# Performance work log

Measured on AMD Instinct MI355X. Metric: run time of the kernel, lower is better.

The kernel has to match this reference:

```python
import jax, jax.numpy as jnp
import numpy as np

H = 8          # number of heads
D_MODEL = 512  # model dim
D_HEAD = D_MODEL // H


def setup_inputs() -> dict:
    key = jax.random.key(0)
    ks = jax.random.split(key, 8)
    B, C, L = 4, D_MODEL, 2048
    s = 1.0 / np.sqrt(D_MODEL)
    return {
        "x1": jax.random.normal(ks[0], (B, C, L), dtype=jnp.float32),
        "x2": jax.random.normal(ks[1], (B, C, L), dtype=jnp.float32),
        "Wq": jax.random.uniform(ks[2], (D_MODEL, D_MODEL), jnp.float32, -s, s),
        "bq": jax.random.uniform(ks[3], (D_MODEL,), jnp.float32, -s, s),
        "Wk": jax.random.uniform(ks[4], (D_MODEL, D_MODEL), jnp.float32, -s, s),
        "bk": jax.random.uniform(ks[5], (D_MODEL,), jnp.float32, -s, s),
        "Wv": jax.random.uniform(ks[6], (D_MODEL, D_MODEL), jnp.float32, -s, s),
        "bv": jax.random.uniform(ks[7], (D_MODEL,), jnp.float32, -s, s),
    }


def reference(x1, x2, Wq, bq, Wk, bk, Wv, bv):
    # x1, x2: [B, C, L] with C == d_model (3D branch of the torch module)
    B, C, L = x1.shape
    x1t = jnp.swapaxes(x1, 1, 2)  # [B, L, C]
    x2t = jnp.swapaxes(x2, 1, 2)  # [B, L, C]

    def proj(x, W, b):  # torch Linear: x @ W.T + b, then split heads
        y = jnp.einsum('blc,dc->bld', x, W) + b          # [B, L, C]
        return y.reshape(B, -1, H, D_HEAD).transpose(0, 2, 1, 3)  # [B, H, L, d]

    q = proj(x1t, Wq, bq)
    k = proj(x2t, Wk, bk)
    v = proj(x2t, Wv, bv)

    scores = jnp.einsum('bhqd,bhkd->bhqk', q, k) / jnp.sqrt(
        jnp.asarray(D_HEAD, dtype=q.dtype))
    attn = jax.nn.softmax(scores, axis=-1)
    out = jnp.einsum('bhqk,bhkd->bhqd', attn, v)          # [B, H, L, d]

    # transpose(1,2).view(B,-1,C).transpose(1,2) -> [B, C, L]
    out = out.transpose(0, 2, 1, 3).reshape(B, L, C)
    return jnp.swapaxes(out, 1, 2)
```

## Files before the change

### kernel.cpp

```cpp
#include <hip/hip_runtime.h>
#include <hip/hip_bf16.h>

#define L_SEQ 2048
#define DM 512
#define NB 4

typedef short bf16x8 __attribute__((ext_vector_type(8)));
typedef float f32x4 __attribute__((ext_vector_type(4)));
typedef unsigned short u16;
typedef u16 u16x8 __attribute__((ext_vector_type(8)));
typedef u16 u16x4 __attribute__((ext_vector_type(4)));

__device__ __forceinline__ u16 f2bf(float f) {
    unsigned int u = __float_as_uint(f);
    u += 0x7fffu + ((u >> 16) & 1u);
    return (u16)(u >> 16);
}

__device__ __forceinline__ unsigned int pk_bf16(float a, float b) {
    __hip_bfloat162 h = __float22bfloat162_rn(float2{a, b});
    unsigned int u;
    __builtin_memcpy(&u, &h, 4);
    return u;
}

__device__ __forceinline__ void lds_load16(const void* g, void* l) {
    __builtin_amdgcn_global_load_lds(
        (const __attribute__((address_space(1))) unsigned int*)g,
        (__attribute__((address_space(3))) unsigned int*)l,
        16, 0, 0);
}

__global__ void cvt_w(const float* __restrict__ Wq, const float* __restrict__ Wk,
                      const float* __restrict__ Wv, u16* __restrict__ dst) {
    int i = blockIdx.x * blockDim.x + threadIdx.x;
    int which = i >> 16, j = i & 65535;
    const float* src = (which == 0) ? Wq : (which == 1 ? Wk : Wv);
    float4 v = ((const float4*)src)[j];
    ushort4 o;
    o.x = f2bf(v.x); o.y = f2bf(v.y); o.z = f2bf(v.z); o.w = f2bf(v.w);
    ((ushort4*)dst)[i] = o;
}

__global__ void tr_cvt_x(const float* __restrict__ x1, const float* __restrict__ x2,
                         u16* __restrict__ dst) {
    __shared__ float t[64][69];
    const int z = blockIdx.z, b = z & 3, c0 = blockIdx.y * 64, l0 = blockIdx.x * 64;
    const float* src = (z < 4) ? x1 : x2;
    u16* dbase = dst + (size_t)(z >> 2) * 4194304;
    const int tid = threadIdx.x;
    const float* sp = src + ((size_t)b * DM + c0) * L_SEQ + l0;
#pragma unroll
    for (int p = 0; p < 4; ++p) {
        int id = p * 256 + tid;
        int ci = id >> 4, lj = (id & 15) * 4;
        float4 v = *(const float4*)(sp + (size_t)ci * L_SEQ + lj);
        t[ci][lj] = v.x; t[ci][lj + 1] = v.y; t[ci][lj + 2] = v.z; t[ci][lj + 3] = v.w;
    }
    __syncthreads();
    u16* dp = dbase + ((size_t)b * L_SEQ + l0) * DM + c0;
#pragma unroll
    for (int p = 0; p < 2; ++p) {
        int id = p * 256 + tid;
        int lj = id >> 3, c8 = (id & 7) * 8;
        u16x8 o;
#pragma unroll
        for (int i = 0; i < 8; ++i) o[i] = f2bf(t[c8 + i][lj]);
        *(u16x8*)(dp + (size_t)lj * DM + c8) = o;
    }
}

__launch_bounds__(256, 2)
__global__ void proj_gemm(const u16* __restrict__ x1T, const u16* __restrict__ x2T,
                          const u16* __restrict__ Wall,
                          const float* __restrict__ bq, const float* __restrict__ bk,
                          const float* __restrict__ bv,
                          u16* __restrict__ Qo, u16* __restrict__ Ko, u16* __restrict__ Vto) {
    __shared__ __align__(16) char smem[34816];
    u16* a_lds = (u16*)smem;
    u16* b_lds = (u16*)(smem + 8192);
    const int by = blockIdx.y;
    const int b = by / 3, pj = by % 3;
    const int m0 = (blockIdx.x >> 2) * 128, n0 = (blockIdx.x & 3) * 128;
    const u16* xT = (pj == 0) ? x1T : x2T;
    const u16* W = Wall + (size_t)pj * 262144;
    const float* bias = (pj == 0) ? bq : (pj == 1 ? bk : bv);
    const float scale = (pj == 0) ? 0.18033688011112042f : 1.0f;

    const int tid = threadIdx.x;
    const int w = tid >> 6, lane = tid & 63;
    const int lm = lane & 15, lq = lane >> 4;
    const int wrow = (w & 1) * 64, wcol = (w >> 1) * 64;

    const u16* gsrc[4];
    u16* ldst[4];
#pragma unroll
    for (int j = 0; j < 4; ++j) {
        int s = (j & 1) * 256 + w * 64 + lane;
        int r = s >> 2, c = s & 3, cc = c ^ (r & 3);
        if (j < 2) {
            gsrc[j] = xT + ((size_t)b * L_SEQ + m0 + r) * DM + cc * 8;
            ldst[j] = a_lds + ((j & 1) * 256 + w * 64) * 8;
        } else {
            gsrc[j] = W + (size_t)(n0 + r) * DM + cc * 8;
            ldst[j] = b_lds + ((j & 1) * 256 + w * 64) * 8;
        }
    }

    f32x4 acc[4][4];
#pragma unroll
    for (int mt = 0; mt < 4; ++mt)
#pragma unroll
        for (int nt = 0; nt < 4; ++nt) acc[mt][nt] = (f32x4){0.f, 0.f, 0.f, 0.f};

    for (int kt = 0; kt < 16; ++kt) {
        __syncthreads();
#pragma unroll
        for (int j = 0; j < 4; ++j) lds_load16(gsrc[j] + kt * 32, ldst[j]);
        __syncthreads();
        bf16x8 af[4], bfr[4];
#pragma unroll
        for (int mt = 0; mt < 4; ++mt) {
            int r = wrow + mt * 16 + lm;
            int ch = lq ^ (r & 3);
            af[mt] = *(const bf16x8*)(a_lds + r * 32 + ch * 8);
        }
#pragma unroll
        for (int nt = 0; nt < 4; ++nt) {
            int r = wcol + nt * 16 + lm;
            int ch = lq ^ (r & 3);
            bfr[nt] = *(const bf16x8*)(b_lds + r * 32 + ch * 8);
        }
#pragma unroll
        for (int mt = 0; mt < 4; ++mt)
#pragma unroll
            for (int nt = 0; nt < 4; ++nt)
                acc[mt][nt] = __builtin_amdgcn_mfma_f32_16x16x32_bf16(af[mt], bfr[nt], acc[mt][nt], 0, 0, 0);
    }

    float bvv[4];
#pragma unroll
    for (int nt = 0; nt < 4; ++nt) bvv[nt] = bias[n0 + wcol + nt * 16 + lm];

    if (pj < 2) {
        u16* dst = (pj == 0) ? Qo : Ko;
#pragma unroll
        for (int mt = 0; mt < 4; ++mt)
#pragma unroll
            for (int nt = 0; nt < 4; ++nt) {
                int col = n0 + wcol + nt * 16 + lm;
#pragma unroll
                for (int r = 0; r < 4; ++r) {
                    int row = m0 + wrow + mt * 16 + lq * 4 + r;
                    dst[((size_t)b * L_SEQ + row) * DM + col] = f2bf((acc[mt][nt][r] + bvv[nt]) * scale);
                }
            }
    } else {
        __syncthreads();
        u16* epi = (u16*)smem;
#pragma unroll
        for (int mt = 0; mt < 4; ++mt)
#pragma unroll
            for (int nt = 0; nt < 4; ++nt) {
                int colL = wcol + nt * 16 + lm;
                int row0 = wrow + mt * 16 + lq * 4;
                u16x4 tv;
#pragma unroll
                for (int r = 0; r < 4; ++r) tv[r] = f2bf(acc[mt][nt][r] + bvv[nt]);
                *(u16x4*)(epi + colL * 136 + row0) = tv;
            }
        __syncthreads();
#pragma unroll
        for (int p = 0; p < 8; ++p) {
            int id = p * 256 + tid;
            int rr = id >> 4, ch = id & 15;
            u16x8 vv = *(const u16x8*)(epi + rr * 136 + ch * 8);
            *(u16x8*)(Vto + ((size_t)b * DM + n0 + rr) * L_SEQ + m0 + ch * 8) = vv;
        }
    }
}

__launch_bounds__(512, 4)
__global__ void attn(const u16* __restrict__ Q, const u16* __restrict__ K,
                     const u16* __restrict__ Vt, float* __restrict__ out) {
    __shared__ __align__(16) char smem[66048];
    u16* k_lds = (u16*)smem;
    u16* v_lds = (u16*)(smem + 16384);
    u16* p_lds = (u16*)(smem + 32768);
    float* o_lds = (float*)(smem + 32768);
    float* l_lds = (float*)(smem + 65536);

    const int qb = blockIdx.x, h = blockIdx.y, b = blockIdx.z;
    const int tid = threadIdx.x, w = tid >> 6, lane = tid & 63;
    const int q0 = qb * 128, wr = w * 16;
    const int lm = lane & 15, lq = lane >> 4;

    const u16* Qb = Q + ((size_t)b * L_SEQ + q0) * DM + h * 64;
    const u16* Kb = K + (size_t)b * L_SEQ * DM + h * 64;
    const u16* Vb = Vt + ((size_t)b * DM + h * 64) * L_SEQ;

    const u16 *gQ[2], *gK[2], *gV[2];
    u16 *dK[2], *dV[2];
#pragma unroll
    for (int j = 0; j < 2; ++j) {
        int s = j * 512 + w * 64 + lane;
        int r = s >> 3, c = s & 7, cc = c ^ (r & 7);
        gQ[j] = Qb + (size_t)r * DM + cc * 8;
        gK[j] = Kb + (size_t)r * DM + cc * 8;
        dK[j] = k_lds + (j * 512 + w * 64) * 8;
        int d = s >> 4, kc = s & 15, kcc = kc ^ (d & 15);
        gV[j] = Vb + (size_t)d * L_SEQ + kcc * 8;
        dV[j] = v_lds + (j * 512 + w * 64) * 8;
    }

#pragma unroll
    for (int j = 0; j < 2; ++j) lds_load16(gQ[j], dK[j]);
    __syncthreads();
    bf16x8 qf[2];
#pragma unroll
    for (int kb = 0; kb < 2; ++kb) {
        int r = wr + lm;
        int ch = (kb * 4 + lq) ^ (r & 7);
        qf[kb] = *(const bf16x8*)(k_lds + r * 64 + ch * 8);
    }

    float l_part = 0.f;
    f32x4 o_acc[4];
#pragma unroll
    for (int dt = 0; dt < 4; ++dt) o_acc[dt] = (f32x4){0.f, 0.f, 0.f, 0.f};

    for (int kt = 0; kt < 16; ++kt) {
        __syncthreads();
#pragma unroll
        for (int j = 0; j < 2; ++j) lds_load16(gK[j] + (size_t)kt * 128 * DM, dK[j]);
#pragma unroll
        for (int j = 0; j < 2; ++j) lds_load16(gV[j] + kt * 128, dV[j]);
        __syncthreads();

#pragma unroll
        for (int nt = 0; nt < 8; ++nt) {
            int rk = nt * 16 + lm;
            bf16x8 kf0 = *(const bf16x8*)(k_lds + rk * 64 + ((0 + lq) ^ (rk & 7)) * 8);
            bf16x8 kf1 = *(const bf16x8*)(k_lds + rk * 64 + ((4 + lq) ^ (rk & 7)) * 8);
            f32x4 s = (f32x4){0.f, 0.f, 0.f, 0.f};
            s = __builtin_amdgcn_mfma_f32_16x16x32_bf16(kf0, qf[0], s, 0, 0, 0);
            s = __builtin_amdgcn_mfma_f32_16x16x32_bf16(kf1, qf[1], s, 0, 0, 0);
            float p0 = __builtin_amdgcn_exp2f(s[0]);
            float p1 = __builtin_amdgcn_exp2f(s[1]);
            float p2 = __builtin_amdgcn_exp2f(s[2]);
            float p3 = __builtin_amdgcn_exp2f(s[3]);
            l_part += (p0 + p1) + (p2 + p3);
            unsigned int w0 = pk_bf16(p0, p1), w1 = pk_bf16(p2, p3);
            int q = wr + lm;
            int c8 = nt * 2 + (lq >> 1);
            int chs = c8 ^ (q & 15);
            uint2 pw; pw.x = w0; pw.y = w1;
            *(uint2*)(p_lds + q * 128 + chs * 8 + (lq & 1) * 4) = pw;
        }

#pragma unroll
        for (int kb = 0; kb < 4; ++kb) {
            int r = wr + lm;
            int ch = (kb * 4 + lq) ^ (r & 15);
            bf16x8 pf = *(const bf16x8*)(p_lds + r * 128 + ch * 8);
#pragma unroll
            for (int dt = 0; dt < 4; ++dt) {
                int d = dt * 16 + lm;
                int chv = (kb * 4 + lq) ^ (d & 15);
                bf16x8 vf = *(const bf16x8*)(v_lds + d * 128 + chv * 8);
                o_acc[dt] = __builtin_amdgcn_mfma_f32_16x16x32_bf16(pf, vf, o_acc[dt], 0, 0, 0);
            }
        }
    }

    l_part += __shfl_xor(l_part, 16);
    l_part += __shfl_xor(l_part, 32);

    __syncthreads();
    if (lq == 0) l_lds[wr + lm] = 1.0f / l_part;
    {
        int row0 = wr + lq * 4;
        int rc = row0 >> 2;
#pragma unroll
        for (int dt = 0; dt < 4; ++dt) {
            int col = dt * 16 + lm;
            *(f32x4*)(o_lds + col * 128 + ((rc ^ (col & 31)) << 2)) = o_acc[dt];
        }
    }
    __syncthreads();
    float* ob = out + ((size_t)b * DM + h * 64) * L_SEQ + q0;
#pragma unroll
    for (int p = 0; p < 4; ++p) {
        int id = p * 512 + tid;
        int d = id >> 5, rc = id & 31;
        f32x4 vv = *(const f32x4*)(o_lds + d * 128 + ((rc ^ (d & 31)) << 2));
        f32x4 il = *(const f32x4*)(l_lds + rc * 4);
#pragma unroll
        for (int j = 0; j < 4; ++j) vv[j] *= il[j];
        *(f32x4*)(ob + (size_t)d * L_SEQ + rc * 4) = vv;
    }
}

extern "C" void kernel_launch(void* const* d_in, const int* in_sizes, int n_in,
                              void* d_out, int out_size, void* d_ws, size_t ws_size,
                              hipStream_t stream) {
    const float* x1 = (const float*)d_in[0];
    const float* x2 = (const float*)d_in[1];
    const float* Wq = (const float*)d_in[2];
    const float* bq = (const float*)d_in[3];
    const float* Wk = (const float*)d_in[4];
    const float* bk = (const float*)d_in[5];
    const float* Wv = (const float*)d_in[6];
    const float* bv = (const float*)d_in[7];
    float* out = (float*)d_out;

    char* ws = (char*)d_ws;
    u16* x1T = (u16*)(ws);
    u16* x2T = (u16*)(ws + 8388608);
    u16* Wall = (u16*)(ws + 16777216);
    u16* Qb  = (u16*)(ws + 18350080);
    u16* Kb  = (u16*)(ws + 26738688);
    u16* Vtb = (u16*)(ws + 35127296);

    cvt_w<<<768, 256, 0, stream>>>(Wq, Wk, Wv, Wall);
    tr_cvt_x<<<dim3(32, 8, 8), 256, 0, stream>>>(x1, x2, x1T);
    proj_gemm<<<dim3(64, 12), 256, 0, stream>>>(x1T, x2T, Wall, bq, bk, bv, Qb, Kb, Vtb);
    attn<<<dim3(16, 8, 4), 512, 0, stream>>>(Qb, Kb, Vtb, out);
}
```

Before: 164.4 us.

## Double-buffer GEMM and attention tiles, stage Q/K epilogue, enlarge transpose tiles

The projection GEMM and the attention kernel now double-buffer their LDS tiles, issuing the next tile's loads before computing on the current one, so each iteration needs one barrier instead of two. Attention switches to 64-key tiles with a smaller LDS footprint and remaps blocks over a linear grid for locality. The Q/K GEMM epilogue goes through LDS to produce coalesced 16-byte stores instead of scattered 2-byte writes. The transpose-convert kernel uses 128x128 tiles and converts to bf16 before staging, which halves shared memory traffic. The cost is more LDS per block and more iterations with shorter bodies in attention, which may affect occupancy and latency hiding.

Measured after the change: 174.6 us. 1.06x slower.

```diff
diff --git a/kernel.cpp b/kernel.cpp
--- a/kernel.cpp
+++ b/kernel.cpp
@@ -3,7 +3,6 @@
 
 #define L_SEQ 2048
 #define DM 512
-#define NB 4
 
 typedef short bf16x8 __attribute__((ext_vector_type(8)));
 typedef float f32x4 __attribute__((ext_vector_type(4)));
@@ -44,41 +43,41 @@
 
 __global__ void tr_cvt_x(const float* __restrict__ x1, const float* __restrict__ x2,
                          u16* __restrict__ dst) {
-    __shared__ float t[64][69];
-    const int z = blockIdx.z, b = z & 3, c0 = blockIdx.y * 64, l0 = blockIdx.x * 64;
+    __shared__ u16 t[128 * 136];
+    const int z = blockIdx.z, b = z & 3, c0 = blockIdx.y * 128, l0 = blockIdx.x * 128;
     const float* src = (z < 4) ? x1 : x2;
     u16* dbase = dst + (size_t)(z >> 2) * 4194304;
     const int tid = threadIdx.x;
     const float* sp = src + ((size_t)b * DM + c0) * L_SEQ + l0;
 #pragma unroll
-    for (int p = 0; p < 4; ++p) {
+    for (int p = 0; p < 16; ++p) {
         int id = p * 256 + tid;
-        int ci = id >> 4, lj = (id & 15) * 4;
-        float4 v = *(const float4*)(sp + (size_t)ci * L_SEQ + lj);
-        t[ci][lj] = v.x; t[ci][lj + 1] = v.y; t[ci][lj + 2] = v.z; t[ci][lj + 3] = v.w;
+        int ci = id >> 5, f4 = id & 31;
+        float4 v = *(const float4*)(sp + (size_t)ci * L_SEQ + f4 * 4);
+        u16x4 o;
+        o[0] = f2bf(v.x); o[1] = f2bf(v.y); o[2] = f2bf(v.z); o[3] = f2bf(v.w);
+        *(u16x4*)(t + ci * 136 + f4 * 4) = o;
     }
     __syncthreads();
     u16* dp = dbase + ((size_t)b * L_SEQ + l0) * DM + c0;
 #pragma unroll
-    for (int p = 0; p < 2; ++p) {
+    for (int p = 0; p < 8; ++p) {
         int id = p * 256 + tid;
-        int lj = id >> 3, c8 = (id & 7) * 8;
+        int lj = id >> 4, c8 = id & 15;
         u16x8 o;
 #pragma unroll
-        for (int i = 0; i < 8; ++i) o[i] = f2bf(t[c8 + i][lj]);
-        *(u16x8*)(dp + (size_t)lj * DM + c8) = o;
-    }
-}
-
-__launch_bounds__(256, 2)
+        for (int i = 0; i < 8; ++i) o[i] = t[(c8 * 8 + i) * 136 + lj];
+        *(u16x8*)(dp + (size_t)lj * DM + c8 * 8) = o;
+    }
+}
+
+__launch_bounds__(256, 3)
 __global__ void proj_gemm(const u16* __restrict__ x1T, const u16* __restrict__ x2T,
                           const u16* __restrict__ Wall,
                           const float* __restrict__ bq, const float* __restrict__ bk,
                           const float* __restrict__ bv,
                           u16* __restrict__ Qo, u16* __restrict__ Ko, u16* __restrict__ Vto) {
     __shared__ __align__(16) char smem[34816];
-    u16* a_lds = (u16*)smem;
-    u16* b_lds = (u16*)(smem + 8192);
     const int by = blockIdx.y;
     const int b = by / 3, pj = by % 3;
     const int m0 = (blockIdx.x >> 2) * 128, n0 = (blockIdx.x & 3) * 128;
@@ -92,19 +91,15 @@
     const int lm = lane & 15, lq = lane >> 4;
     const int wrow = (w & 1) * 64, wcol = (w >> 1) * 64;
 
-    const u16* gsrc[4];
-    u16* ldst[4];
-#pragma unroll
-    for (int j = 0; j < 4; ++j) {
-        int s = (j & 1) * 256 + w * 64 + lane;
+    const u16* gA[2]; const u16* gB[2];
+    int adst[2];
+#pragma unroll
+    for (int j = 0; j < 2; ++j) {
+        int s = j * 256 + tid;
         int r = s >> 2, c = s & 3, cc = c ^ (r & 3);
-        if (j < 2) {
-            gsrc[j] = xT + ((size_t)b * L_SEQ + m0 + r) * DM + cc * 8;
-            ldst[j] = a_lds + ((j & 1) * 256 + w * 64) * 8;
-        } else {
-            gsrc[j] = W + (size_t)(n0 + r) * DM + cc * 8;
-            ldst[j] = b_lds + ((j & 1) * 256 + w * 64) * 8;
-        }
+        gA[j] = xT + ((size_t)b * L_SEQ + m0 + r) * DM + cc * 8;
+        gB[j] = W + (size_t)(n0 + r) * DM + cc * 8;
+        adst[j] = (j * 256 + w * 64) * 8;
     }
 
     f32x4 acc[4][4];
@@ -112,24 +107,35 @@
     for (int mt = 0; mt < 4; ++mt)
 #pragma unroll
         for (int nt = 0; nt < 4; ++nt) acc[mt][nt] = (f32x4){0.f, 0.f, 0.f, 0.f};
+
+#pragma unroll
+    for (int j = 0; j < 2; ++j) {
+        lds_load16(gA[j], (u16*)smem + adst[j]);
+        lds_load16(gB[j], (u16*)(smem + 8192) + adst[j]);
+    }
 
     for (int kt = 0; kt < 16; ++kt) {
         __syncthreads();
-#pragma unroll
-        for (int j = 0; j < 4; ++j) lds_load16(gsrc[j] + kt * 32, ldst[j]);
-        __syncthreads();
+        if (kt < 15) {
+            int nb = (kt + 1) & 1;
+#pragma unroll
+            for (int j = 0; j < 2; ++j) {
+                lds_load16(gA[j] + (kt + 1) * 32, (u16*)(smem + nb * 16384) + adst[j]);
+                lds_load16(gB[j] + (kt + 1) * 32, (u16*)(smem + 8192 + nb * 16384) + adst[j]);
+            }
+        }
+        const u16* a_lds = (const u16*)(smem + (kt & 1) * 16384);
+        const u16* b_lds = (const u16*)(smem + 8192 + (kt & 1) * 16384);
         bf16x8 af[4], bfr[4];
 #pragma unroll
         for (int mt = 0; mt < 4; ++mt) {
             int r = wrow + mt * 16 + lm;
-            int ch = lq ^ (r & 3);
-            af[mt] = *(const bf16x8*)(a_lds + r * 32 + ch * 8);
+            af[mt] = *(const bf16x8*)(a_lds + r * 32 + (lq ^ (r & 3)) * 8);
         }
 #pragma unroll
         for (int nt = 0; nt < 4; ++nt) {
             int r = wcol + nt * 16 + lm;
-            int ch = lq ^ (r & 3);
-            bfr[nt] = *(const bf16x8*)(b_lds + r * 32 + ch * 8);
+            bfr[nt] = *(const bf16x8*)(b_lds + r * 32 + (lq ^ (r & 3)) * 8);
         }
 #pragma unroll
         for (int mt = 0; mt < 4; ++mt)
@@ -142,34 +148,32 @@
 #pragma unroll
     for (int nt = 0; nt < 4; ++nt) bvv[nt] = bias[n0 + wcol + nt * 16 + lm];
 
+    __syncthreads();
+    u16* epi = (u16*)smem;
+#pragma unroll
+    for (int mt = 0; mt < 4; ++mt)
+#pragma unroll
+        for (int nt = 0; nt < 4; ++nt) {
+            int colL = wcol + nt * 16 + lm;
+            int row0 = wrow + mt * 16 + lq * 4;
+            u16x4 tv;
+#pragma unroll
+            for (int r = 0; r < 4; ++r) tv[r] = f2bf((acc[mt][nt][r] + bvv[nt]) * scale);
+            *(u16x4*)(epi + colL * 136 + row0) = tv;
+        }
+    __syncthreads();
     if (pj < 2) {
         u16* dst = (pj == 0) ? Qo : Ko;
 #pragma unroll
-        for (int mt = 0; mt < 4; ++mt)
-#pragma unroll
-            for (int nt = 0; nt < 4; ++nt) {
-                int col = n0 + wcol + nt * 16 + lm;
-#pragma unroll
-                for (int r = 0; r < 4; ++r) {
-                    int row = m0 + wrow + mt * 16 + lq * 4 + r;
-                    dst[((size_t)b * L_SEQ + row) * DM + col] = f2bf((acc[mt][nt][r] + bvv[nt]) * scale);
-                }
-            }
+        for (int p = 0; p < 8; ++p) {
+            int id = p * 256 + tid;
+            int lj = id >> 4, c8 = id & 15;
+            u16x8 o;
+#pragma unroll
+            for (int i = 0; i < 8; ++i) o[i] = epi[(c8 * 8 + i) * 136 + lj];
+            *(u16x8*)(dst + ((size_t)b * L_SEQ + m0 + lj) * DM + n0 + c8 * 8) = o;
+        }
     } else {
-        __syncthreads();
-        u16* epi = (u16*)smem;
-#pragma unroll
-        for (int mt = 0; mt < 4; ++mt)
-#pragma unroll
-            for (int nt = 0; nt < 4; ++nt) {
-                int colL = wcol + nt * 16 + lm;
-                int row0 = wrow + mt * 16 + lq * 4;
-                u16x4 tv;
-#pragma unroll
-                for (int r = 0; r < 4; ++r) tv[r] = f2bf(acc[mt][nt][r] + bvv[nt]);
-                *(u16x4*)(epi + colL * 136 + row0) = tv;
-            }
-        __syncthreads();
 #pragma unroll
         for (int p = 0; p < 8; ++p) {
             int id = p * 256 + tid;
@@ -183,14 +187,16 @@
 __launch_bounds__(512, 4)
 __global__ void attn(const u16* __restrict__ Q, const u16* __restrict__ K,
                      const u16* __restrict__ Vt, float* __restrict__ out) {
-    __shared__ __align__(16) char smem[66048];
-    u16* k_lds = (u16*)smem;
-    u16* v_lds = (u16*)(smem + 16384);
+    __shared__ __align__(16) char smem[49664];
     u16* p_lds = (u16*)(smem + 32768);
-    float* o_lds = (float*)(smem + 32768);
-    float* l_lds = (float*)(smem + 65536);
-
-    const int qb = blockIdx.x, h = blockIdx.y, b = blockIdx.z;
+    float* l_lds = (float*)(smem + 49152);
+    float* o_lds = (float*)smem;
+
+    const int i = blockIdx.x;
+    const int g = i & 7, r_ = i >> 3;
+    const int qb = r_ & 15, bh = ((r_ >> 4) << 3) + g;
+    const int h = bh >> 2, b = bh & 3;
+
     const int tid = threadIdx.x, w = tid >> 6, lane = tid & 63;
     const int q0 = qb * 128, wr = w * 16;
     const int lm = lane & 15, lq = lane >> 4;
@@ -199,49 +205,55 @@
     const u16* Kb = K + (size_t)b * L_SEQ * DM + h * 64;
     const u16* Vb = Vt + ((size_t)b * DM + h * 64) * L_SEQ;
 
-    const u16 *gQ[2], *gK[2], *gV[2];
-    u16 *dK[2], *dV[2];
+    const u16 *gK, *gV;
+    int sdst;
+    {
+        int r = tid >> 3, c = tid & 7, cc = c ^ (r & 7);
+        gK = Kb + (size_t)r * DM + cc * 8;
+        gV = Vb + (size_t)r * L_SEQ + cc * 8;
+        sdst = (w * 64) * 8;
+    }
+
 #pragma unroll
     for (int j = 0; j < 2; ++j) {
-        int s = j * 512 + w * 64 + lane;
+        int s = j * 512 + tid;
         int r = s >> 3, c = s & 7, cc = c ^ (r & 7);
-        gQ[j] = Qb + (size_t)r * DM + cc * 8;
-        gK[j] = Kb + (size_t)r * DM + cc * 8;
-        dK[j] = k_lds + (j * 512 + w * 64) * 8;
-        int d = s >> 4, kc = s & 15, kcc = kc ^ (d & 15);
-        gV[j] = Vb + (size_t)d * L_SEQ + kcc * 8;
-        dV[j] = v_lds + (j * 512 + w * 64) * 8;
-    }
-
-#pragma unroll
-    for (int j = 0; j < 2; ++j) lds_load16(gQ[j], dK[j]);
+        lds_load16(Qb + (size_t)r * DM + cc * 8, (u16*)(smem + j * 8192) + sdst);
+    }
     __syncthreads();
     bf16x8 qf[2];
 #pragma unroll
     for (int kb = 0; kb < 2; ++kb) {
         int r = wr + lm;
-        int ch = (kb * 4 + lq) ^ (r & 7);
-        qf[kb] = *(const bf16x8*)(k_lds + r * 64 + ch * 8);
-    }
+        const u16* qsrc = (const u16*)(smem + (r >> 6) * 8192)
+                          + (r & 63) * 64 + ((kb * 4 + lq) ^ (r & 7)) * 8;
+        qf[kb] = *(const bf16x8*)qsrc;
+    }
+    __syncthreads();
 
     float l_part = 0.f;
     f32x4 o_acc[4];
 #pragma unroll
     for (int dt = 0; dt < 4; ++dt) o_acc[dt] = (f32x4){0.f, 0.f, 0.f, 0.f};
 
-    for (int kt = 0; kt < 16; ++kt) {
+    lds_load16(gK, (u16*)smem + sdst);
+    lds_load16(gV, (u16*)(smem + 16384) + sdst);
+
+    for (int kt = 0; kt < 32; ++kt) {
         __syncthreads();
-#pragma unroll
-        for (int j = 0; j < 2; ++j) lds_load16(gK[j] + (size_t)kt * 128 * DM, dK[j]);
-#pragma unroll
-        for (int j = 0; j < 2; ++j) lds_load16(gV[j] + kt * 128, dV[j]);
-        __syncthreads();
-
-#pragma unroll
-        for (int nt = 0; nt < 8; ++nt) {
+        if (kt < 31) {
+            int nb = (kt + 1) & 1;
+            lds_load16(gK + (size_t)(kt + 1) * 64 * DM, (u16*)(smem + nb * 8192) + sdst);
+            lds_load16(gV + (kt + 1) * 64, (u16*)(smem + 16384 + nb * 8192) + sdst);
+        }
+        const u16* kl = (const u16*)(smem + (kt & 1) * 8192);
+        const u16* vl = (const u16*)(smem + 16384 + (kt & 1) * 8192);
+
+#pragma unroll
+        for (int nt = 0; nt < 4; ++nt) {
             int rk = nt * 16 + lm;
-            bf16x8 kf0 = *(const bf16x8*)(k_lds + rk * 64 + ((0 + lq) ^ (rk & 7)) * 8);
-            bf16x8 kf1 = *(const bf16x8*)(k_lds + rk * 64 + ((4 + lq) ^ (rk & 7)) * 8);
+            bf16x8 kf0 = *(const bf16x8*)(kl + rk * 64 + ((0 + lq) ^ (rk & 7)) * 8);
+            bf16x8 kf1 = *(const bf16x8*)(kl + rk * 64 + ((4 + lq) ^ (rk & 7)) * 8);
             f32x4 s = (f32x4){0.f, 0.f, 0.f, 0.f};
             s = __builtin_amdgcn_mfma_f32_16x16x32_bf16(kf0, qf[0], s, 0, 0, 0);
             s = __builtin_amdgcn_mfma_f32_16x16x32_bf16(kf1, qf[1], s, 0, 0, 0);
@@ -253,21 +265,19 @@
             unsigned int w0 = pk_bf16(p0, p1), w1 = pk_bf16(p2, p3);
             int q = wr + lm;
             int c8 = nt * 2 + (lq >> 1);
-            int chs = c8 ^ (q & 15);
+            int chs = c8 ^ (q & 7);
             uint2 pw; pw.x = w0; pw.y = w1;
-            *(uint2*)(p_lds + q * 128 + chs * 8 + (lq & 1) * 4) = pw;
-        }
-
-#pragma unroll
-        for (int kb = 0; kb < 4; ++kb) {
+            *(uint2*)(p_lds + q * 64 + chs * 8 + (lq & 1) * 4) = pw;
+        }
+
+#pragma unroll
+        for (int kb = 0; kb < 2; ++kb) {
             int r = wr + lm;
-            int ch = (kb * 4 + lq) ^ (r & 15);
-            bf16x8 pf = *(const bf16x8*)(p_lds + r * 128 + ch * 8);
+            bf16x8 pf = *(const bf16x8*)(p_lds + r * 64 + ((kb * 4 + lq) ^ (r & 7)) * 8);
 #pragma unroll
             for (int dt = 0; dt < 4; ++dt) {
                 int d = dt * 16 + lm;
-                int chv = (kb * 4 + lq) ^ (d & 15);
-                bf16x8 vf = *(const bf16x8*)(v_lds + d * 128 + chv * 8);
+                bf16x8 vf = *(const bf16x8*)(vl + d * 64 + ((kb * 4 + lq) ^ (d & 7)) * 8);
                 o_acc[dt] = __builtin_amdgcn_mfma_f32_16x16x32_bf16(pf, vf, o_acc[dt], 0, 0, 0);
             }
         }
@@ -279,8 +289,7 @@
     __syncthreads();
     if (lq == 0) l_lds[wr + lm] = 1.0f / l_part;
     {
-        int row0 = wr + lq * 4;
-        int rc = row0 >> 2;
+        int rc = w * 4 + lq;
 #pragma unroll
         for (int dt = 0; dt < 4; ++dt) {
             int col = dt * 16 + lm;
@@ -323,7 +332,7 @@
     u16* Vtb = (u16*)(ws + 35127296);
 
     cvt_w<<<768, 256, 0, stream>>>(Wq, Wk, Wv, Wall);
-    tr_cvt_x<<<dim3(32, 8, 8), 256, 0, stream>>>(x1, x2, x1T);
+    tr_cvt_x<<<dim3(16, 4, 8), 256, 0, stream>>>(x1, x2, x1T);
     proj_gemm<<<dim3(64, 12), 256, 0, stream>>>(x1T, x2T, Wall, bq, bk, bv, Qb, Kb, Vtb);
-    attn<<<dim3(16, 8, 4), 512, 0, stream>>>(Qb, Kb, Vtb, out);
-}
+    attn<<<512, 512, 0, stream>>>(Qb, Kb, Vtb, out);
+}
```
